# Optimization experiments

Measured on AMD Instinct MI355X. Metric: run time of the kernel, lower is better.

The kernel has to match this reference:

```python
import jax, jax.numpy as jnp
import numpy as np
from jax import lax

K = 7  # kernel_size
PAD = K // 2


def _feature_difference(t):
    # t: [B, C, H, W] -> normalized census-style local differences [B, K*K, H, W]
    intensity = t.mean(axis=1, keepdims=True)  # [B,1,H,W]
    # Equivalent to conv2d with the identity (eye) kernel in the torch module:
    # channel k gathers the neighbor at offset (k//K, k%K) with zero padding.
    patches = lax.conv_general_dilated_patches(
        intensity, filter_shape=(K, K), window_strides=(1, 1),
        padding=[(PAD, PAD), (PAD, PAD)])  # [B, K*K, H, W]
    local_diff = patches - intensity
    return local_diff / jnp.sqrt(0.81 + local_diff * local_diff)


def setup_inputs() -> dict:
    key = jax.random.key(0)
    kx, ky = jax.random.split(key)
    B, C, H, W = 8, 3, 320, 1024
    x = jax.random.uniform(kx, (B, C, H, W), dtype=jnp.float32)
    y = jax.random.uniform(ky, (B, C, H, W), dtype=jnp.float32)
    return {"x": x, "y": y}


def reference(x, y):
    diff_x = _feature_difference(x)
    diff_y = _feature_difference(y)
    diff_total = diff_x - lax.stop_gradient(diff_y)  # .detach() on y branch
    d2 = diff_total * diff_total
    dist = (d2 / (0.1 + d2)).mean(axis=1, keepdims=True)  # [B,1,H,W]
    b, c, h, w = x.shape
    # valid-region mask: ones in the interior, zeros in the PAD-wide border
    mask = jnp.zeros((b, 1, h, w), dtype=x.dtype)
    mask = mask.at[:, :, PAD:h - PAD, PAD:w - PAD].set(1.0)
    return (dist * mask).mean()
```

## Files before the change

kernel.cpp:

```cpp
#include <hip/hip_runtime.h>

typedef float f32x2 __attribute__((ext_vector_type(2)));
typedef float f32x4 __attribute__((ext_vector_type(4)));

#define PAD 3
#define HH 320
#define WW 1024
#define BB 8
#define TH 32
#define TW 64
#define LDS_W  72
#define NF4    (LDS_W/4)
#define RPW 8
#define NWAVES 4
#define NTHREADS 256
#define WROWS (RPW + 6)
#define NPOSW (WROWS * NF4)

#define NIN ((HH - 2*PAD) * (WW - 2*PAD))
#define OUT_SCALE (1.0 / (49.0 * (double)BB * (double)HH * (double)WW))
#define C0 ((float)(48.0 * (double)BB * (double)NIN * OUT_SCALE))
#define NEG_SCALE ((float)(-0.1 * OUT_SCALE))

#define KEEP(v) asm("" : "+v"(v))

static __device__ __forceinline__ f32x2 mk2(float a, float b){ f32x2 r; r.x=a; r.y=b; return r; }
static __device__ __forceinline__ f32x2 sp2(float a){ f32x2 r; r.x=a; r.y=a; return r; }
static __device__ __forceinline__ f32x2 fma2(f32x2 a, f32x2 b, f32x2 c){
    return __builtin_elementwise_fma(a, b, c);
}

template<bool INTERIOR>
static __device__ __forceinline__ void pair2(f32x2 nx, f32x2 ny, f32x2 cx2, f32x2 cy2,
                                             f32x2 w2, float& acc)
{
    f32x2 dx  = nx - cx2;
    f32x2 dy  = ny - cy2;
    f32x2 dx2 = dx * dx;
    f32x2 dy2 = dy * dy;
    f32x2 ax  = dx2 + sp2(0.81f);
    f32x2 ay  = dy2 + sp2(0.81f);
    f32x2 P   = ax * ay;
    f32x2 s; s.x = __builtin_amdgcn_rsqf(P.x); s.y = __builtin_amdgcn_rsqf(P.y);
    f32x2 A   = fma2(dx2, ay, dy2 * ax);
    f32x2 h   = dx * dy;
    f32x2 inner = fma2(s, A, h * sp2(-2.0f));
    f32x2 t2  = s * inner;
    f32x2 den = t2 + sp2(0.1f);
    float ip  = __builtin_amdgcn_rcpf(den.x * den.y);
    float cross;
    if constexpr (INTERIOR) cross = den.x + den.y;
    else                    cross = fmaf(w2.x, den.y, w2.y * den.x);
    acc = fmaf(ip, cross, acc);
}

template<bool INTERIOR>
static __device__ __forceinline__ float compute_rows(
    const float (&sx)[WROWS][LDS_W], const float (&sy)[WROWS][LDS_W],
    int tile_i, int tile_j, int tx, int li0)
{
    float cO3 = 0.0f;
    f32x2 cP0 = {}, cP1 = {}, cP2 = {}, cP3 = {};
    if constexpr (!INTERIOR) {
        float cO[7];
        const int gj = tile_j + tx;
        #pragma unroll
        for (int d = 0; d < 7; ++d) {
            int nj = gj + d - 3;
            cO[d] = (nj >= PAD && nj < WW - PAD) ? 1.0f : 0.0f;
        }
        cP0 = mk2(cO[0], cO[1]);
        cP1 = mk2(cO[2], cO[3]);
        cP2 = mk2(cO[4], cO[5]);
        cP3 = sp2(cO[6]);
        cO3 = cO[3];
    }

    float wx[4][7], wy[4][7];
    #pragma unroll
    for (int r = 0; r < 3; ++r) {
        #pragma unroll
        for (int d = 0; d < 7; ++d) {
            float a = sx[3 + r][tx + 1 + d]; KEEP(a); wx[r][d] = a;
            float c = sy[3 + r][tx + 1 + d]; KEEP(c); wy[r][d] = c;
        }
    }

    float acc = 0.0f;

    #pragma unroll 1
    for (int io = 0; io < RPW / 4; ++io) {
        #pragma unroll
        for (int iu = 0; iu < 4; ++iu) {
            const int lr = io * 4 + iu;
            const int gi = tile_i + li0 + lr;
            const int sn = (iu + 3) & 3;
            #pragma unroll
            for (int d = 0; d < 7; ++d) {
                float a = sx[lr + 6][tx + 1 + d]; KEEP(a); wx[sn][d] = a;
                float c = sy[lr + 6][tx + 1 + d]; KEEP(c); wy[sn][d] = c;
            }

            float rin[4] = {};
            f32x2 mc2 = {};
            if constexpr (!INTERIOR) {
                #pragma unroll
                for (int di = 0; di < 4; ++di) {
                    int ni = gi + di;
                    rin[di] = (ni >= PAD && ni < HH - PAD) ? 1.0f : 0.0f;
                }
                mc2 = sp2(rin[0] * cO3);
            }

            const int s0 = iu & 3, s1 = (iu+1)&3, s2 = (iu+2)&3, s3_ = (iu+3)&3;
            const f32x2 cx2 = sp2(wx[s0][3]);
            const f32x2 cy2 = sp2(wy[s0][3]);

            pair2<INTERIOR>(mk2(wx[s0][4], wx[s0][5]), mk2(wy[s0][4], wy[s0][5]),
                cx2, cy2, INTERIOR ? sp2(0.0f) : fma2(sp2(rin[0]), cP2, mc2), acc);

            #pragma unroll
            for (int di = 1; di <= 3; ++di) {
                const int s = (iu + di) & 3;
                const f32x2 rin2 = sp2(rin[di]);
                pair2<INTERIOR>(mk2(wx[s][0], wx[s][1]), mk2(wy[s][0], wy[s][1]),
                    cx2, cy2, INTERIOR ? sp2(0.0f) : fma2(rin2, cP0, mc2), acc);
                pair2<INTERIOR>(mk2(wx[s][2], wx[s][3]), mk2(wy[s][2], wy[s][3]),
                    cx2, cy2, INTERIOR ? sp2(0.0f) : fma2(rin2, cP1, mc2), acc);
                pair2<INTERIOR>(mk2(wx[s][4], wx[s][5]), mk2(wy[s][4], wy[s][5]),
                    cx2, cy2, INTERIOR ? sp2(0.0f) : fma2(rin2, cP2, mc2), acc);
            }

            pair2<INTERIOR>(mk2(wx[s0][6], wx[s1][6]), mk2(wy[s0][6], wy[s1][6]),
                cx2, cy2, INTERIOR ? sp2(0.0f) : fma2(mk2(rin[0], rin[1]), cP3, mc2), acc);
            pair2<INTERIOR>(mk2(wx[s2][6], wx[s3_][6]), mk2(wy[s2][6], wy[s3_][6]),
                cx2, cy2, INTERIOR ? sp2(0.0f) : fma2(mk2(rin[2], rin[3]), cP3, mc2), acc);
        }
    }

    return acc;
}

__global__ __launch_bounds__(NTHREADS, 4) void ternary_loss_kernel(
    const float* __restrict__ x, const float* __restrict__ y,
    float* __restrict__ out)
{
    __shared__ __align__(16) float sIx[NWAVES][WROWS][LDS_W];
    __shared__ __align__(16) float sIy[NWAVES][WROWS][LDS_W];
    __shared__ float wave_sums[NWAVES];

    const int tile_j = blockIdx.x * TW;
    const int tile_i = blockIdx.y * TH;
    const int b      = blockIdx.z;
    const int tx  = threadIdx.x;
    const int wv  = threadIdx.y;
    const int tid = wv * 64 + tx;

    const size_t PLANE = (size_t)HH * WW;
    const float* xb = x + (size_t)b * 3 * PLANE;
    const float* yb = y + (size_t)b * 3 * PLANE;

    const int li0 = wv * RPW;

    for (int p = tx; p < NPOSW; p += 64) {
        int r  = p / NF4;
        int c4 = p - r * NF4;
        int gi  = tile_i + li0 - 3 + r;
        int gj0 = tile_j - 4 + 4 * c4;
        f32x4 vx = {0.0f, 0.0f, 0.0f, 0.0f};
        f32x4 vy = {0.0f, 0.0f, 0.0f, 0.0f};
        if ((unsigned)gi < (unsigned)HH && (unsigned)gj0 < (unsigned)WW) {
            const float* px = xb + (size_t)gi * WW + gj0;
            f32x4 a0 = *(const f32x4*)(px);
            f32x4 a1 = *(const f32x4*)(px + PLANE);
            f32x4 a2 = *(const f32x4*)(px + 2 * PLANE);
            vx = (a0 + a1 + a2) * (1.0f / 3.0f);
            const float* py = yb + (size_t)gi * WW + gj0;
            f32x4 b0 = *(const f32x4*)(py);
            f32x4 b1 = *(const f32x4*)(py + PLANE);
            f32x4 b2 = *(const f32x4*)(py + 2 * PLANE);
            vy = (b0 + b1 + b2) * (1.0f / 3.0f);
        }
        *(f32x4*)&sIx[wv][r][4 * c4] = vx;
        *(f32x4*)&sIy[wv][r][4 * c4] = vy;
    }

    const bool interior = (tile_i >= PAD) && (tile_i + TH + PAD <= HH - PAD)
                       && (tile_j >= 2*PAD) && (tile_j + TW + PAD <= WW - PAD);

    float acc;
    if (interior)
        acc = 2.0f * compute_rows<true >(sIx[wv], sIy[wv], tile_i, tile_j, tx, li0);
    else
        acc =        compute_rows<false>(sIx[wv], sIy[wv], tile_i, tile_j, tx, li0);

    #pragma unroll
    for (int off = 32; off > 0; off >>= 1)
        acc += __shfl_down(acc, off, 64);
    if (tx == 0) wave_sums[wv] = acc;
    __syncthreads();
    if (tid == 0) {
        float total = (wave_sums[0] + wave_sums[1] + wave_sums[2] + wave_sums[3]) * NEG_SCALE;
        if (blockIdx.x == 0 && blockIdx.y == 0 && blockIdx.z == 0)
            total += C0;
        atomicAdd(out, total);
    }
}

extern "C" void kernel_launch(void* const* d_in, const int* in_sizes, int n_in,
                              void* d_out, int out_size, void* d_ws, size_t ws_size,
                              hipStream_t stream) {
    const float* x = (const float*)d_in[0];
    const float* y = (const float*)d_in[1];
    float* out = (float*)d_out;

    hipMemsetAsync(out, 0, sizeof(float), stream);

    dim3 grid(WW / TW, HH / TH, BB);
    dim3 block(64, NWAVES, 1);
    ternary_loss_kernel<<<grid, block, 0, stream>>>(x, y, out);
}
```

Baseline: 119.3 us.

## Share block-wide halo tile and pipeline global loads with per-row compute

Replaces per-wave private halo buffers (each wave loading 14 rows, with overlapping halos) with one shared 38-row block tile. Rows are now interleaved across waves, and each phase prefetches the next 4 halo rows from global memory into registers while the current row is computed, then stores them to LDS and synchronizes. This cuts redundant global loads and LDS footprint and hides load latency behind compute. In exchange it adds a block barrier per phase, drops the rolling register window so each row reloads 4x7 values from LDS, and leaves only 120 of the 256 threads doing loads.

```diff
diff --git a/kernel.cpp b/kernel.cpp
--- a/kernel.cpp
+++ b/kernel.cpp
@@ -9,13 +9,16 @@
 #define BB 8
 #define TH 32
 #define TW 64
+#define HALO_H (TH + 2*PAD)
 #define LDS_W  72
 #define NF4    (LDS_W/4)
-#define RPW 8
 #define NWAVES 4
 #define NTHREADS 256
-#define WROWS (RPW + 6)
-#define NPOSW (WROWS * NF4)
+#define PRO_ROWS 10
+#define NPOS_PRO (PRO_ROWS * NF4)
+#define GROUP_ROWS 4
+#define NPOS_G (GROUP_ROWS * NF4)
+#define NPHASE 8
 
 #define NIN ((HH - 2*PAD) * (WW - 2*PAD))
 #define OUT_SCALE (1.0 / (49.0 * (double)BB * (double)HH * (double)WW))
@@ -54,11 +57,40 @@
     acc = fmaf(ip, cross, acc);
 }
 
+static __device__ __forceinline__ void stage_pos(
+    float (&sIx)[HALO_H][LDS_W], float (&sIy)[HALO_H][LDS_W],
+    const float* __restrict__ xb, const float* __restrict__ yb,
+    int tile_i, int tile_j, int r, int c4)
+{
+    const size_t PLANE = (size_t)HH * WW;
+    int gi  = tile_i - PAD + r;
+    int gj0 = tile_j - 4 + 4 * c4;
+    f32x4 vx = {0.0f, 0.0f, 0.0f, 0.0f};
+    f32x4 vy = {0.0f, 0.0f, 0.0f, 0.0f};
+    if ((unsigned)gi < (unsigned)HH && (unsigned)gj0 < (unsigned)WW) {
+        const float* px = xb + (size_t)gi * WW + gj0;
+        f32x4 a0 = *(const f32x4*)(px);
+        f32x4 a1 = *(const f32x4*)(px + PLANE);
+        f32x4 a2 = *(const f32x4*)(px + 2 * PLANE);
+        vx = (a0 + a1 + a2) * (1.0f / 3.0f);
+        const float* py = yb + (size_t)gi * WW + gj0;
+        f32x4 b0 = *(const f32x4*)(py);
+        f32x4 b1 = *(const f32x4*)(py + PLANE);
+        f32x4 b2 = *(const f32x4*)(py + 2 * PLANE);
+        vy = (b0 + b1 + b2) * (1.0f / 3.0f);
+    }
+    *(f32x4*)&sIx[r][4 * c4] = vx;
+    *(f32x4*)&sIy[r][4 * c4] = vy;
+}
+
 template<bool INTERIOR>
-static __device__ __forceinline__ float compute_rows(
-    const float (&sx)[WROWS][LDS_W], const float (&sy)[WROWS][LDS_W],
-    int tile_i, int tile_j, int tx, int li0)
-{
+static __device__ __forceinline__ float run_phases(
+    float (&sIx)[HALO_H][LDS_W], float (&sIy)[HALO_H][LDS_W],
+    const float* __restrict__ xb, const float* __restrict__ yb,
+    int tile_i, int tile_j, int tx, int wv, int tid)
+{
+    const size_t PLANE = (size_t)HH * WW;
+
     float cO3 = 0.0f;
     f32x2 cP0 = {}, cP1 = {}, cP2 = {}, cP3 = {};
     if constexpr (!INTERIOR) {
@@ -76,29 +108,45 @@
         cO3 = cO[3];
     }
 
-    float wx[4][7], wy[4][7];
-    #pragma unroll
-    for (int r = 0; r < 3; ++r) {
-        #pragma unroll
-        for (int d = 0; d < 7; ++d) {
-            float a = sx[3 + r][tx + 1 + d]; KEEP(a); wx[r][d] = a;
-            float c = sy[3 + r][tx + 1 + d]; KEEP(c); wy[r][d] = c;
-        }
-    }
-
     float acc = 0.0f;
 
     #pragma unroll 1
-    for (int io = 0; io < RPW / 4; ++io) {
-        #pragma unroll
-        for (int iu = 0; iu < 4; ++iu) {
-            const int lr = io * 4 + iu;
-            const int gi = tile_i + li0 + lr;
-            const int sn = (iu + 3) & 3;
+    for (int p = 0; p < NPHASE; ++p) {
+        f32x4 a0{}, a1{}, a2{}, b0{}, b1{}, b2{};
+        float mB = 0.0f;
+        int hr = 0, cb4 = 0;
+        const bool doSt = (p < NPHASE - 1) && (tid < NPOS_G);
+        if (doSt) {
+            hr  = PRO_ROWS + GROUP_ROWS * p + tid / NF4;
+            cb4 = tid - (tid / NF4) * NF4;
+            int gi  = tile_i - PAD + hr;
+            int gj0 = tile_j - 4 + 4 * cb4;
+            bool ok = ((unsigned)gi < (unsigned)HH) && ((unsigned)gj0 < (unsigned)WW);
+            size_t off = ok ? ((size_t)gi * WW + gj0) : 0;
+            const float* px = xb + off;
+            const float* py = yb + off;
+            a0 = *(const f32x4*)(px);
+            a1 = *(const f32x4*)(px + PLANE);
+            a2 = *(const f32x4*)(px + 2 * PLANE);
+            b0 = *(const f32x4*)(py);
+            b1 = *(const f32x4*)(py + PLANE);
+            b2 = *(const f32x4*)(py + 2 * PLANE);
+            mB = ok ? (1.0f / 3.0f) : 0.0f;
+        }
+        __builtin_amdgcn_sched_barrier(0);
+
+        {
+            const int R  = GROUP_ROWS * p + wv;
+            const int gi = tile_i + R;
+
+            float wx[4][7], wy[4][7];
             #pragma unroll
-            for (int d = 0; d < 7; ++d) {
-                float a = sx[lr + 6][tx + 1 + d]; KEEP(a); wx[sn][d] = a;
-                float c = sy[lr + 6][tx + 1 + d]; KEEP(c); wy[sn][d] = c;
+            for (int di = 0; di < 4; ++di) {
+                #pragma unroll
+                for (int d = 0; d < 7; ++d) {
+                    float A_ = sIx[R + 3 + di][tx + 1 + d]; KEEP(A_); wx[di][d] = A_;
+                    float C_ = sIy[R + 3 + di][tx + 1 + d]; KEEP(C_); wy[di][d] = C_;
+                }
             }
 
             float rin[4] = {};
@@ -112,30 +160,37 @@
                 mc2 = sp2(rin[0] * cO3);
             }
 
-            const int s0 = iu & 3, s1 = (iu+1)&3, s2 = (iu+2)&3, s3_ = (iu+3)&3;
-            const f32x2 cx2 = sp2(wx[s0][3]);
-            const f32x2 cy2 = sp2(wy[s0][3]);
-
-            pair2<INTERIOR>(mk2(wx[s0][4], wx[s0][5]), mk2(wy[s0][4], wy[s0][5]),
+            const f32x2 cx2 = sp2(wx[0][3]);
+            const f32x2 cy2 = sp2(wy[0][3]);
+
+            pair2<INTERIOR>(mk2(wx[0][4], wx[0][5]), mk2(wy[0][4], wy[0][5]),
                 cx2, cy2, INTERIOR ? sp2(0.0f) : fma2(sp2(rin[0]), cP2, mc2), acc);
 
             #pragma unroll
             for (int di = 1; di <= 3; ++di) {
-                const int s = (iu + di) & 3;
                 const f32x2 rin2 = sp2(rin[di]);
-                pair2<INTERIOR>(mk2(wx[s][0], wx[s][1]), mk2(wy[s][0], wy[s][1]),
+                pair2<INTERIOR>(mk2(wx[di][0], wx[di][1]), mk2(wy[di][0], wy[di][1]),
                     cx2, cy2, INTERIOR ? sp2(0.0f) : fma2(rin2, cP0, mc2), acc);
-                pair2<INTERIOR>(mk2(wx[s][2], wx[s][3]), mk2(wy[s][2], wy[s][3]),
+                pair2<INTERIOR>(mk2(wx[di][2], wx[di][3]), mk2(wy[di][2], wy[di][3]),
                     cx2, cy2, INTERIOR ? sp2(0.0f) : fma2(rin2, cP1, mc2), acc);
-                pair2<INTERIOR>(mk2(wx[s][4], wx[s][5]), mk2(wy[s][4], wy[s][5]),
+                pair2<INTERIOR>(mk2(wx[di][4], wx[di][5]), mk2(wy[di][4], wy[di][5]),
                     cx2, cy2, INTERIOR ? sp2(0.0f) : fma2(rin2, cP2, mc2), acc);
             }
 
-            pair2<INTERIOR>(mk2(wx[s0][6], wx[s1][6]), mk2(wy[s0][6], wy[s1][6]),
+            pair2<INTERIOR>(mk2(wx[0][6], wx[1][6]), mk2(wy[0][6], wy[1][6]),
                 cx2, cy2, INTERIOR ? sp2(0.0f) : fma2(mk2(rin[0], rin[1]), cP3, mc2), acc);
-            pair2<INTERIOR>(mk2(wx[s2][6], wx[s3_][6]), mk2(wy[s2][6], wy[s3_][6]),
+            pair2<INTERIOR>(mk2(wx[2][6], wx[3][6]), mk2(wy[2][6], wy[3][6]),
                 cx2, cy2, INTERIOR ? sp2(0.0f) : fma2(mk2(rin[2], rin[3]), cP3, mc2), acc);
         }
+        __builtin_amdgcn_sched_barrier(0);
+
+        if (doSt) {
+            f32x4 vx = (a0 + a1 + a2) * mB;
+            f32x4 vy = (b0 + b1 + b2) * mB;
+            *(f32x4*)&sIx[hr][4 * cb4] = vx;
+            *(f32x4*)&sIy[hr][4 * cb4] = vy;
+        }
+        __syncthreads();
     }
 
     return acc;
@@ -145,8 +200,8 @@
     const float* __restrict__ x, const float* __restrict__ y,
     float* __restrict__ out)
 {
-    __shared__ __align__(16) float sIx[NWAVES][WROWS][LDS_W];
-    __shared__ __align__(16) float sIy[NWAVES][WROWS][LDS_W];
+    __shared__ __align__(16) float sIx[HALO_H][LDS_W];
+    __shared__ __align__(16) float sIy[HALO_H][LDS_W];
     __shared__ float wave_sums[NWAVES];
 
     const int tile_j = blockIdx.x * TW;
@@ -160,39 +215,21 @@
     const float* xb = x + (size_t)b * 3 * PLANE;
     const float* yb = y + (size_t)b * 3 * PLANE;
 
-    const int li0 = wv * RPW;
-
-    for (int p = tx; p < NPOSW; p += 64) {
+    for (int p = tid; p < NPOS_PRO; p += NTHREADS) {
         int r  = p / NF4;
         int c4 = p - r * NF4;
-        int gi  = tile_i + li0 - 3 + r;
-        int gj0 = tile_j - 4 + 4 * c4;
-        f32x4 vx = {0.0f, 0.0f, 0.0f, 0.0f};
-        f32x4 vy = {0.0f, 0.0f, 0.0f, 0.0f};
-        if ((unsigned)gi < (unsigned)HH && (unsigned)gj0 < (unsigned)WW) {
-            const float* px = xb + (size_t)gi * WW + gj0;
-            f32x4 a0 = *(const f32x4*)(px);
-            f32x4 a1 = *(const f32x4*)(px + PLANE);
-            f32x4 a2 = *(const f32x4*)(px + 2 * PLANE);
-            vx = (a0 + a1 + a2) * (1.0f / 3.0f);
-            const float* py = yb + (size_t)gi * WW + gj0;
-            f32x4 b0 = *(const f32x4*)(py);
-            f32x4 b1 = *(const f32x4*)(py + PLANE);
-            f32x4 b2 = *(const f32x4*)(py + 2 * PLANE);
-            vy = (b0 + b1 + b2) * (1.0f / 3.0f);
-        }
-        *(f32x4*)&sIx[wv][r][4 * c4] = vx;
-        *(f32x4*)&sIy[wv][r][4 * c4] = vy;
-    }
+        stage_pos(sIx, sIy, xb, yb, tile_i, tile_j, r, c4);
+    }
+    __syncthreads();
 
     const bool interior = (tile_i >= PAD) && (tile_i + TH + PAD <= HH - PAD)
                        && (tile_j >= 2*PAD) && (tile_j + TW + PAD <= WW - PAD);
 
     float acc;
     if (interior)
-        acc = 2.0f * compute_rows<true >(sIx[wv], sIy[wv], tile_i, tile_j, tx, li0);
+        acc = 2.0f * run_phases<true >(sIx, sIy, xb, yb, tile_i, tile_j, tx, wv, tid);
     else
-        acc =        compute_rows<false>(sIx[wv], sIy[wv], tile_i, tile_j, tx, li0);
+        acc =        run_phases<false>(sIx, sIy, xb, yb, tile_i, tile_j, tx, wv, tid);
 
     #pragma unroll
     for (int off = 32; off > 0; off >>= 1)
```

New measurement: 120.3 us. Within noise of the previous version (+0.8%).

## Share halo tile across waves and batch reciprocals over four neighbor terms

Applied to the files above, without the earlier changes.

Replaces per-wave LDS halo tiles with a single block-wide halo tile loaded cooperatively by all threads, removing redundant global loads and channel averaging of overlapping halo rows, at the cost of a block barrier. Restructures the loss accumulation so one reciprocal covers the combined fraction of two pairs (four neighbor terms), halving transcendental reciprocal instructions at the cost of extra multiplies and slightly different rounding.

```diff
diff --git a/kernel.cpp b/kernel.cpp
--- a/kernel.cpp
+++ b/kernel.cpp
@@ -9,13 +9,13 @@
 #define BB 8
 #define TH 32
 #define TW 64
+#define HALO_H (TH + 2*PAD)
 #define LDS_W  72
 #define NF4    (LDS_W/4)
+#define NPOS   (HALO_H * NF4)
 #define RPW 8
 #define NWAVES 4
 #define NTHREADS 256
-#define WROWS (RPW + 6)
-#define NPOSW (WROWS * NF4)
 
 #define NIN ((HH - 2*PAD) * (WW - 2*PAD))
 #define OUT_SCALE (1.0 / (49.0 * (double)BB * (double)HH * (double)WW))
@@ -30,9 +30,7 @@
     return __builtin_elementwise_fma(a, b, c);
 }
 
-template<bool INTERIOR>
-static __device__ __forceinline__ void pair2(f32x2 nx, f32x2 ny, f32x2 cx2, f32x2 cy2,
-                                             f32x2 w2, float& acc)
+static __device__ __forceinline__ f32x2 den2(f32x2 nx, f32x2 ny, f32x2 cx2, f32x2 cy2)
 {
     f32x2 dx  = nx - cx2;
     f32x2 dy  = ny - cy2;
@@ -45,19 +43,27 @@
     f32x2 A   = fma2(dx2, ay, dy2 * ax);
     f32x2 h   = dx * dy;
     f32x2 inner = fma2(s, A, h * sp2(-2.0f));
-    f32x2 t2  = s * inner;
-    f32x2 den = t2 + sp2(0.1f);
-    float ip  = __builtin_amdgcn_rcpf(den.x * den.y);
-    float cross;
-    if constexpr (INTERIOR) cross = den.x + den.y;
-    else                    cross = fmaf(w2.x, den.y, w2.y * den.x);
-    acc = fmaf(ip, cross, acc);
+    return fma2(s, inner, sp2(0.1f));
+}
+
+template<bool INTERIOR>
+static __device__ __forceinline__ void comb4(f32x2 a, f32x2 b, f32x2 wa, f32x2 wb,
+                                             float& acc)
+{
+    float Pa = a.x * a.y;
+    float Pb = b.x * b.y;
+    float ca, cb;
+    if constexpr (INTERIOR) { ca = a.x + a.y;                 cb = b.x + b.y; }
+    else { ca = fmaf(wa.x, a.y, wa.y * a.x);  cb = fmaf(wb.x, b.y, wb.y * b.x); }
+    float Q = Pa * Pb;
+    float C = fmaf(ca, Pb, cb * Pa);
+    acc = fmaf(C, __builtin_amdgcn_rcpf(Q), acc);
 }
 
 template<bool INTERIOR>
 static __device__ __forceinline__ float compute_rows(
-    const float (&sx)[WROWS][LDS_W], const float (&sy)[WROWS][LDS_W],
-    int tile_i, int tile_j, int tx, int li0)
+    const float (&sIx)[HALO_H][LDS_W], const float (&sIy)[HALO_H][LDS_W],
+    int tile_i, int tile_j, int tx, int wv)
 {
     float cO3 = 0.0f;
     f32x2 cP0 = {}, cP1 = {}, cP2 = {}, cP3 = {};
@@ -76,13 +82,15 @@
         cO3 = cO[3];
     }
 
+    const int li0 = wv * RPW;
+
     float wx[4][7], wy[4][7];
     #pragma unroll
     for (int r = 0; r < 3; ++r) {
         #pragma unroll
         for (int d = 0; d < 7; ++d) {
-            float a = sx[3 + r][tx + 1 + d]; KEEP(a); wx[r][d] = a;
-            float c = sy[3 + r][tx + 1 + d]; KEEP(c); wy[r][d] = c;
+            float a = sIx[li0 + 3 + r][tx + 1 + d]; KEEP(a); wx[r][d] = a;
+            float c = sIy[li0 + 3 + r][tx + 1 + d]; KEEP(c); wy[r][d] = c;
         }
     }
 
@@ -92,13 +100,13 @@
     for (int io = 0; io < RPW / 4; ++io) {
         #pragma unroll
         for (int iu = 0; iu < 4; ++iu) {
-            const int lr = io * 4 + iu;
-            const int gi = tile_i + li0 + lr;
+            const int li = li0 + io * 4 + iu;
+            const int gi = tile_i + li;
             const int sn = (iu + 3) & 3;
             #pragma unroll
             for (int d = 0; d < 7; ++d) {
-                float a = sx[lr + 6][tx + 1 + d]; KEEP(a); wx[sn][d] = a;
-                float c = sy[lr + 6][tx + 1 + d]; KEEP(c); wy[sn][d] = c;
+                float a = sIx[li + 6][tx + 1 + d]; KEEP(a); wx[sn][d] = a;
+                float c = sIy[li + 6][tx + 1 + d]; KEEP(c); wy[sn][d] = c;
             }
 
             float rin[4] = {};
@@ -116,25 +124,43 @@
             const f32x2 cx2 = sp2(wx[s0][3]);
             const f32x2 cy2 = sp2(wy[s0][3]);
 
-            pair2<INTERIOR>(mk2(wx[s0][4], wx[s0][5]), mk2(wy[s0][4], wy[s0][5]),
-                cx2, cy2, INTERIOR ? sp2(0.0f) : fma2(sp2(rin[0]), cP2, mc2), acc);
-
-            #pragma unroll
-            for (int di = 1; di <= 3; ++di) {
-                const int s = (iu + di) & 3;
-                const f32x2 rin2 = sp2(rin[di]);
-                pair2<INTERIOR>(mk2(wx[s][0], wx[s][1]), mk2(wy[s][0], wy[s][1]),
-                    cx2, cy2, INTERIOR ? sp2(0.0f) : fma2(rin2, cP0, mc2), acc);
-                pair2<INTERIOR>(mk2(wx[s][2], wx[s][3]), mk2(wy[s][2], wy[s][3]),
-                    cx2, cy2, INTERIOR ? sp2(0.0f) : fma2(rin2, cP1, mc2), acc);
-                pair2<INTERIOR>(mk2(wx[s][4], wx[s][5]), mk2(wy[s][4], wy[s][5]),
-                    cx2, cy2, INTERIOR ? sp2(0.0f) : fma2(rin2, cP2, mc2), acc);
+            f32x2 d0  = den2(mk2(wx[s0][4], wx[s0][5]), mk2(wy[s0][4], wy[s0][5]), cx2, cy2);
+            f32x2 d1  = den2(mk2(wx[s1][0], wx[s1][1]), mk2(wy[s1][0], wy[s1][1]), cx2, cy2);
+            f32x2 d2  = den2(mk2(wx[s1][2], wx[s1][3]), mk2(wy[s1][2], wy[s1][3]), cx2, cy2);
+            f32x2 d3  = den2(mk2(wx[s1][4], wx[s1][5]), mk2(wy[s1][4], wy[s1][5]), cx2, cy2);
+            f32x2 d4  = den2(mk2(wx[s2][0], wx[s2][1]), mk2(wy[s2][0], wy[s2][1]), cx2, cy2);
+            f32x2 d5  = den2(mk2(wx[s2][2], wx[s2][3]), mk2(wy[s2][2], wy[s2][3]), cx2, cy2);
+            f32x2 d6  = den2(mk2(wx[s2][4], wx[s2][5]), mk2(wy[s2][4], wy[s2][5]), cx2, cy2);
+            f32x2 d7  = den2(mk2(wx[s3_][0], wx[s3_][1]), mk2(wy[s3_][0], wy[s3_][1]), cx2, cy2);
+            f32x2 d8  = den2(mk2(wx[s3_][2], wx[s3_][3]), mk2(wy[s3_][2], wy[s3_][3]), cx2, cy2);
+            f32x2 d9  = den2(mk2(wx[s3_][4], wx[s3_][5]), mk2(wy[s3_][4], wy[s3_][5]), cx2, cy2);
+            f32x2 d10 = den2(mk2(wx[s0][6], wx[s1][6]),  mk2(wy[s0][6], wy[s1][6]),  cx2, cy2);
+            f32x2 d11 = den2(mk2(wx[s2][6], wx[s3_][6]), mk2(wy[s2][6], wy[s3_][6]), cx2, cy2);
+
+            f32x2 W0 = {}, W1 = {}, W2 = {}, W3 = {}, W4 = {}, W5 = {};
+            f32x2 W6 = {}, W7 = {}, W8 = {}, W9 = {}, W10 = {}, W11 = {};
+            if constexpr (!INTERIOR) {
+                const f32x2 r1v = sp2(rin[1]), r2v = sp2(rin[2]), r3v = sp2(rin[3]);
+                W0  = fma2(sp2(rin[0]), cP2, mc2);
+                W1  = fma2(r1v, cP0, mc2);
+                W2  = fma2(r1v, cP1, mc2);
+                W3  = fma2(r1v, cP2, mc2);
+                W4  = fma2(r2v, cP0, mc2);
+                W5  = fma2(r2v, cP1, mc2);
+                W6  = fma2(r2v, cP2, mc2);
+                W7  = fma2(r3v, cP0, mc2);
+                W8  = fma2(r3v, cP1, mc2);
+                W9  = fma2(r3v, cP2, mc2);
+                W10 = fma2(mk2(rin[0], rin[1]), cP3, mc2);
+                W11 = fma2(mk2(rin[2], rin[3]), cP3, mc2);
             }
 
-            pair2<INTERIOR>(mk2(wx[s0][6], wx[s1][6]), mk2(wy[s0][6], wy[s1][6]),
-                cx2, cy2, INTERIOR ? sp2(0.0f) : fma2(mk2(rin[0], rin[1]), cP3, mc2), acc);
-            pair2<INTERIOR>(mk2(wx[s2][6], wx[s3_][6]), mk2(wy[s2][6], wy[s3_][6]),
-                cx2, cy2, INTERIOR ? sp2(0.0f) : fma2(mk2(rin[2], rin[3]), cP3, mc2), acc);
+            comb4<INTERIOR>(d0,  d1,  W0,  W1,  acc);
+            comb4<INTERIOR>(d2,  d3,  W2,  W3,  acc);
+            comb4<INTERIOR>(d4,  d5,  W4,  W5,  acc);
+            comb4<INTERIOR>(d6,  d7,  W6,  W7,  acc);
+            comb4<INTERIOR>(d8,  d9,  W8,  W9,  acc);
+            comb4<INTERIOR>(d10, d11, W10, W11, acc);
         }
     }
 
@@ -145,8 +171,8 @@
     const float* __restrict__ x, const float* __restrict__ y,
     float* __restrict__ out)
 {
-    __shared__ __align__(16) float sIx[NWAVES][WROWS][LDS_W];
-    __shared__ __align__(16) float sIy[NWAVES][WROWS][LDS_W];
+    __shared__ __align__(16) float sIx[HALO_H][LDS_W];
+    __shared__ __align__(16) float sIy[HALO_H][LDS_W];
     __shared__ float wave_sums[NWAVES];
 
     const int tile_j = blockIdx.x * TW;
@@ -160,12 +186,10 @@
     const float* xb = x + (size_t)b * 3 * PLANE;
     const float* yb = y + (size_t)b * 3 * PLANE;
 
-    const int li0 = wv * RPW;
-
-    for (int p = tx; p < NPOSW; p += 64) {
+    for (int p = tid; p < NPOS; p += NTHREADS) {
         int r  = p / NF4;
         int c4 = p - r * NF4;
-        int gi  = tile_i + li0 - 3 + r;
+        int gi  = tile_i - PAD + r;
         int gj0 = tile_j - 4 + 4 * c4;
         f32x4 vx = {0.0f, 0.0f, 0.0f, 0.0f};
         f32x4 vy = {0.0f, 0.0f, 0.0f, 0.0f};
@@ -181,18 +205,17 @@
             f32x4 b2 = *(const f32x4*)(py + 2 * PLANE);
             vy = (b0 + b1 + b2) * (1.0f / 3.0f);
         }
-        *(f32x4*)&sIx[wv][r][4 * c4] = vx;
-        *(f32x4*)&sIy[wv][r][4 * c4] = vy;
-    }
+        *(f32x4*)&sIx[r][4 * c4] = vx;
+        *(f32x4*)&sIy[r][4 * c4] = vy;
+    }
+    __syncthreads();
 
     const bool interior = (tile_i >= PAD) && (tile_i + TH + PAD <= HH - PAD)
                        && (tile_j >= 2*PAD) && (tile_j + TW + PAD <= WW - PAD);
 
     float acc;
-    if (interior)
-        acc = 2.0f * compute_rows<true >(sIx[wv], sIy[wv], tile_i, tile_j, tx, li0);
-    else
-        acc =        compute_rows<false>(sIx[wv], sIy[wv], tile_i, tile_j, tx, li0);
+    if (interior) acc = 2.0f * compute_rows<true >(sIx, sIy, tile_i, tile_j, tx, wv);
+    else          acc =        compute_rows<false>(sIx, sIy, tile_i, tile_j, tx, wv);
 
     #pragma unroll
     for (int off = 32; off > 0; off >>= 1)
```

After: 119.9 us. No clear change (+0.5%).
